# Kernel optimization log

Hardware: AMD Instinct MI355X
Metric: run time of the kernel (lower is better)

## Reference

```python
import jax, jax.numpy as jnp
import numpy as np

D_MODEL = 2048
N_HEADS = 16
N_KV_HEADS = 4
HEAD_DIM = D_MODEL // N_HEADS
KV_DIM = N_KV_HEADS * HEAD_DIM
EPS = 1e-6


def setup_inputs() -> dict:
    key = jax.random.key(0)
    ks = jax.random.split(key, 5)
    N, L = 4, 2048
    x = jax.random.normal(ks[0], (N, L, D_MODEL), dtype=jnp.float32)
    Wqkv = jax.random.normal(ks[1], (D_MODEL, D_MODEL + 2 * KV_DIM), dtype=jnp.float32) * (1.0 / np.sqrt(D_MODEL))
    bqkv = jnp.zeros((D_MODEL + 2 * KV_DIM,), dtype=jnp.float32)
    Wout = jax.random.normal(ks[2], (D_MODEL, D_MODEL), dtype=jnp.float32) * (1.0 / np.sqrt(D_MODEL))
    bout = jnp.zeros((D_MODEL,), dtype=jnp.float32)
    q_scale = jnp.ones((HEAD_DIM,), dtype=jnp.float32)
    k_scale = jnp.ones((HEAD_DIM,), dtype=jnp.float32)
    return {"x": x, "Wqkv": Wqkv, "bqkv": bqkv, "q_scale": q_scale, "k_scale": k_scale, "Wout": Wout, "bout": bout}


def _rmsnorm(x, scale):
    return x * (scale / jnp.sqrt(jnp.mean(jnp.square(x), axis=-1, keepdims=True) + EPS))


def reference(x, Wqkv, bqkv, q_scale, k_scale, Wout, bout):
    N, L, D = x.shape
    qkv = x @ Wqkv + bqkv  # [N, L, D + 2*kv_dim]
    q = qkv[..., :D].reshape(N, L, N_HEADS, HEAD_DIM).transpose(0, 2, 1, 3)          # [N,H,L,hd]
    k = qkv[..., D:D + KV_DIM].reshape(N, L, N_KV_HEADS, HEAD_DIM).transpose(0, 2, 1, 3)  # [N,Hkv,L,hd]
    v = qkv[..., D + KV_DIM:].reshape(N, L, N_KV_HEADS, HEAD_DIM).transpose(0, 2, 1, 3)
    q = _rmsnorm(q, q_scale)
    k = _rmsnorm(k, k_scale)
    # GQA expand (repeat_interleave over head dim)
    n_rep = N_HEADS // N_KV_HEADS
    k = jnp.repeat(k, n_rep, axis=1)
    v = jnp.repeat(v, n_rep, axis=1)
    scale = 1.0 / jnp.sqrt(jnp.float32(HEAD_DIM))
    scores = jnp.einsum("nhqd,nhkd->nhqk", q, k) * scale  # [N,H,L,L]
    causal = jnp.tril(jnp.ones((L, L), dtype=bool))
    scores = jnp.where(causal, scores, jnp.finfo(scores.dtype).min)
    attn = jax.nn.softmax(scores, axis=-1)
    y = jnp.einsum("nhqk,nhkd->nhqd", attn, v)  # [N,H,L,hd]
    y = y.transpose(0, 2, 1, 3).reshape(N, L, D)
    return y @ Wout + bout
```

## Files before the change

### kernel.cpp

```cpp
#include <hip/hip_runtime.h>

typedef unsigned int uint_t;
typedef unsigned short ushort_t;

using f32x4 = __attribute__((ext_vector_type(4))) float;
using bf16x8 = __attribute__((ext_vector_type(8))) short;

#define D_MODEL 2048
#define N_HEADS 16
#define N_KV    4
#define HD      128
#define KV_DIM  (N_KV * HD)
#define NQKV    (D_MODEL + 2*KV_DIM)
#define SEQ     2048
#define NB      4
#define MROWS   (NB * SEQ)
#define SM_SCALE 0.08838834764831845f

__device__ __forceinline__ ushort_t f2bf(float f) {
    uint_t u = __float_as_uint(f);
    u = (u + 0x7FFFu + ((u >> 16) & 1u)) >> 16;
    return (ushort_t)u;
}

__device__ __forceinline__ void gload16(const ushort_t* g, ushort_t* l) {
    __builtin_amdgcn_global_load_lds(
        (const __attribute__((address_space(1))) unsigned int*)g,
        (__attribute__((address_space(3))) unsigned int*)l, 16, 0, 0);
}

__global__ __launch_bounds__(256) void conv_x_kernel(const float* __restrict__ in,
                                                     ushort_t* __restrict__ out, int n) {
    int i = (blockIdx.x * 256 + threadIdx.x) * 4;
    if (i >= n) return;
    float4 v = *(const float4*)&in[i];
    ushort_t o[4] = {f2bf(v.x), f2bf(v.y), f2bf(v.z), f2bf(v.w)};
    *(uint2*)&out[i] = *(uint2*)o;
}

__global__ __launch_bounds__(256) void conv_wt_kernel(const float* __restrict__ W,
                                                      ushort_t* __restrict__ WT,
                                                      int K, int Nout) {
    __shared__ float tile[32][33];
    int n0 = blockIdx.x * 32, k0 = blockIdx.y * 32;
    int tx = threadIdx.x, ty = threadIdx.y;
    for (int i = 0; i < 4; ++i)
        tile[ty + 8*i][tx] = W[(size_t)(k0 + ty + 8*i) * Nout + n0 + tx];
    __syncthreads();
    for (int i = 0; i < 4; ++i)
        WT[(size_t)(n0 + ty + 8*i) * K + k0 + tx] = f2bf(tile[tx][ty + 8*i]);
}

#define GEMM_STAGE(A, BT, k0, b)                                                   \
    for (int i = 0; i < 4; ++i) {                                                  \
        int ci = (w * 4 + i) * 64 + lane;                                          \
        int row = ci >> 3, c = ci & 7, cg = c ^ (row & 7);                         \
        gload16(&A [(size_t)(bm + row) * K + (k0) + cg * 8], &As[b][0][0] + (w * 4 + i) * 512); \
        gload16(&BT[(size_t)(bn + row) * K + (k0) + cg * 8], &Bs[b][0][0] + (w * 4 + i) * 512); \
    }

#define GEMM_MAIN_LOOP(A, BT, K)                                                   \
    GEMM_STAGE(A, BT, 0, 0)                                                        \
    {                                                                              \
        int buf = 0;                                                               \
        for (int k0 = 0; k0 < K; k0 += 64) {                                       \
            __syncthreads();                     \
            if (k0 + 64 < K) { GEMM_STAGE(A, BT, k0 + 64, buf ^ 1) }               \
            for (int kk = 0; kk < 64; kk += 32) {                                  \
                bf16x8 af[4], bfr[4];                                              \
                int k4 = kk >> 3;                                                  \
                for (int i = 0; i < 4; ++i)                                        \
                    af[i]  = *(const bf16x8*)&As[buf][mb + i * 16 + r][((k4 + quad) ^ (r & 7)) * 8]; \
                for (int j = 0; j < 4; ++j)                                        \
                    bfr[j] = *(const bf16x8*)&Bs[buf][nb + j * 16 + r][((k4 + quad) ^ (r & 7)) * 8]; \
                for (int i = 0; i < 4; ++i)                                        \
                    for (int j = 0; j < 4; ++j)                                    \
                        acc[i][j] = __builtin_amdgcn_mfma_f32_16x16x32_bf16(af[i], bfr[j], acc[i][j], 0, 0, 0); \
            }                                                                      \
            buf ^= 1;                                                              \
        }                                                                          \
    }

__global__ __launch_bounds__(256) void gemm_bt_kernel(const ushort_t* __restrict__ A,
                                                      const ushort_t* __restrict__ BT,
                                                      const float* __restrict__ bias,
                                                      float* __restrict__ C,
                                                      int M, int N, int K) {
    __shared__ ushort_t As[2][128][64];
    __shared__ ushort_t Bs[2][128][64];
    const int bm = blockIdx.x * 128, bn = blockIdx.y * 128;
    const int t = threadIdx.x;
    const int w = t >> 6, lane = t & 63, quad = lane >> 4, r = lane & 15;
    const int mb = (w >> 1) * 64, nb = (w & 1) * 64;
    f32x4 acc[4][4] = {};
    GEMM_MAIN_LOOP(A, BT, K)
    for (int i = 0; i < 4; ++i)
        for (int j = 0; j < 4; ++j)
            for (int reg = 0; reg < 4; ++reg) {
                int row = bm + mb + i * 16 + quad * 4 + reg;
                int col = bn + nb + j * 16 + r;
                C[(size_t)row * N + col] = acc[i][j][reg] + bias[col];
            }
}

__global__ __launch_bounds__(256) void gemm_qkv_kernel(const ushort_t* __restrict__ A,
                                                       const ushort_t* __restrict__ BT,
                                                       const float* __restrict__ bias,
                                                       const float* __restrict__ q_scale,
                                                       const float* __restrict__ k_scale,
                                                       ushort_t* __restrict__ Q,
                                                       ushort_t* __restrict__ Kb,
                                                       ushort_t* __restrict__ Vt) {
    __shared__ ushort_t As[2][128][64];
    __shared__ ushort_t Bs[2][128][64];
    const int K = D_MODEL;
    const int bm = blockIdx.x * 128, bn = blockIdx.y * 128;
    const int t = threadIdx.x;
    const int w = t >> 6, lane = t & 63, quad = lane >> 4, r = lane & 15;
    const int mb = (w >> 1) * 64, nb = (w & 1) * 64;
    f32x4 acc[4][4] = {};
    GEMM_MAIN_LOOP(A, BT, K)

    const int g = blockIdx.y;
    float bj[4];
    for (int j = 0; j < 4; ++j) bj[j] = bias[bn + nb + j * 16 + r];
    for (int i = 0; i < 4; ++i)
        for (int j = 0; j < 4; ++j)
            for (int reg = 0; reg < 4; ++reg) acc[i][j][reg] += bj[j];

    const int n = bm >> 11, lb = bm & 2047;
    if (g < 20) {
        __syncthreads();
        float* ssum = (float*)&As[0][0][0];
        for (int i = 0; i < 4; ++i)
            for (int reg = 0; reg < 4; ++reg) {
                float p = 0.f;
                for (int j = 0; j < 4; ++j) p += acc[i][j][reg] * acc[i][j][reg];
                p += __shfl_xor(p, 1); p += __shfl_xor(p, 2);
                p += __shfl_xor(p, 4); p += __shfl_xor(p, 8);
                if (r == 0) ssum[(w & 1) * 128 + mb + i * 16 + quad * 4 + reg] = p;
            }
        __syncthreads();
        const float* scp = (g < 16) ? q_scale : k_scale;
        const float smul = (g < 16) ? SM_SCALE : 1.0f;
        float scj[4];
        for (int j = 0; j < 4; ++j) scj[j] = scp[nb + j * 16 + r];
        ushort_t* dst = (g < 16) ? (Q  + (size_t)(n * 16 + g) * SEQ * HD)
                                 : (Kb + (size_t)(n * 4 + g - 16) * SEQ * HD);
        for (int i = 0; i < 4; ++i)
            for (int reg = 0; reg < 4; ++reg) {
                int rl = mb + i * 16 + quad * 4 + reg;
                float ss = ssum[rl] + ssum[128 + rl];
                float iv = rsqrtf(ss * (1.0f / 128.0f) + 1e-6f) * smul;
                size_t lrow = lb + rl;
                for (int j = 0; j < 4; ++j) {
                    int d = nb + j * 16 + r;
                    dst[lrow * HD + d] = f2bf(acc[i][j][reg] * iv * scj[j]);
                }
            }
    } else {
        ushort_t* dstT = Vt + (size_t)(n * 4 + g - 20) * HD * SEQ;
        for (int i = 0; i < 4; ++i)
            for (int j = 0; j < 4; ++j) {
                int d = nb + j * 16 + r;
                ushort_t o[4];
                for (int reg = 0; reg < 4; ++reg) o[reg] = f2bf(acc[i][j][reg]);
                *(uint2*)&dstT[(size_t)d * SEQ + lb + mb + i * 16 + quad * 4] = *(uint2*)o;
            }
    }
}

__global__ __launch_bounds__(256, 2) void attn_kernel(const ushort_t* __restrict__ Q,
                                                      const ushort_t* __restrict__ K,
                                                      const ushort_t* __restrict__ Vt,
                                                      ushort_t* __restrict__ Y) {
    const int pid = blockIdx.x, h = blockIdx.y, n = blockIdx.z;
    const int kvh = h >> 2;
    const ushort_t* Qp = Q  + (size_t)(n * N_HEADS + h) * SEQ * HD;
    const ushort_t* Kp = K  + (size_t)(n * N_KV + kvh) * SEQ * HD;
    const ushort_t* Vp = Vt + (size_t)(n * N_KV + kvh) * HD * SEQ;

    __shared__ ushort_t Ks[2][64][128];
    __shared__ ushort_t Vts[2][128][64];
    __shared__ ushort_t Ps[128][64];

    const int t = threadIdx.x, w = t >> 6, lane = t & 63, quad = lane >> 4, r = lane & 15;

#define ATTN_STAGE(ct, b)                                                           \
    for (int i = 0; i < 4; ++i) {                                                   \
        int ci = (w * 4 + i) * 64 + lane;                                           \
        {                                         \
            int row = ci >> 4, c = ci & 15, cg = c ^ (row & 7);                     \
            gload16(&Kp[(size_t)((ct) * 64 + row) * HD + cg * 8],                   \
                    &Ks[b][0][0] + (w * 4 + i) * 512);                              \
        }                                                                           \
        {                                         \
            int row = ci >> 3, c = ci & 7, cg = c ^ (row & 7);                      \
            gload16(&Vp[(size_t)row * SEQ + (ct) * 64 + cg * 8],                    \
                    &Vts[b][0][0] + (w * 4 + i) * 512);                             \
        }                                                                           \
    }

    for (int rep = 0; rep < 2; ++rep) {
        const int qt = rep ? (15 - pid) : pid;
        const int q0 = qt * 128;

        __syncthreads();
        ATTN_STAGE(0, 0)

        bf16x8 aq[2][4];
        for (int s = 0; s < 2; ++s)
            for (int kc = 0; kc < 4; ++kc)
                aq[s][kc] = *(const bf16x8*)&Qp[(size_t)(q0 + w * 32 + s * 16 + r) * HD + kc * 32 + quad * 8];

        f32x4 oacc[2][8] = {};
        float lsum[2][4] = {};
        const int nct = 2 * qt + 2;
        int buf = 0;

        for (int ct = 0; ct < nct; ++ct) {
            __syncthreads();
            if (ct + 1 < nct) { ATTN_STAGE(ct + 1, buf ^ 1) }

            if (ct * 64 <= q0 + w * 32 + 31) {
                f32x4 sacc[2][4] = {};
                for (int kc = 0; kc < 4; ++kc)
                    for (int jt = 0; jt < 4; ++jt) {
                        bf16x8 bk = *(const bf16x8*)&Ks[buf][jt * 16 + r][((kc * 4 + quad) ^ (r & 7)) * 8];
                        sacc[0][jt] = __builtin_amdgcn_mfma_f32_16x16x32_bf16(aq[0][kc], bk, sacc[0][jt], 0, 0, 0);
                        sacc[1][jt] = __builtin_amdgcn_mfma_f32_16x16x32_bf16(aq[1][kc], bk, sacc[1][jt], 0, 0, 0);
                    }

                const bool diag = (ct >= 2 * qt);
                for (int s = 0; s < 2; ++s)
                    for (int reg = 0; reg < 4; ++reg) {
                        int prow = w * 32 + s * 16 + quad * 4 + reg;
                        int qg = q0 + prow;
                        float rs = 0.f;
                        for (int jt = 0; jt < 4; ++jt) {
                            float sv = sacc[s][jt][reg];
                            if (diag && (ct * 64 + jt * 16 + r) > qg) sv = -1e30f;
                            float p = __expf(sv);
                            rs += p;
                            int colp = ((((jt * 2 + (r >> 3)) ^ prow) & 7) << 3) | (r & 7);
                            Ps[prow][colp] = (ushort_t)(__float_as_uint(p) >> 16);
                        }
                        lsum[s][reg] += rs;
                    }

                for (int kk = 0; kk < 64; kk += 32) {
                    bf16x8 pa[2];
                    for (int s = 0; s < 2; ++s) {
                        int row = w * 32 + s * 16 + r;
                        pa[s] = *(const bf16x8*)&Ps[row][((((kk >> 3) + quad) ^ row) & 7) * 8];
                    }
                    for (int dt = 0; dt < 8; ++dt) {
                        bf16x8 bv = *(const bf16x8*)&Vts[buf][dt * 16 + r][((((kk >> 3) + quad) ^ (r & 7)) & 7) * 8];
                        oacc[0][dt] = __builtin_amdgcn_mfma_f32_16x16x32_bf16(pa[0], bv, oacc[0][dt], 0, 0, 0);
                        oacc[1][dt] = __builtin_amdgcn_mfma_f32_16x16x32_bf16(pa[1], bv, oacc[1][dt], 0, 0, 0);
                    }
                }
            }
            buf ^= 1;
        }

        for (int s = 0; s < 2; ++s)
            for (int reg = 0; reg < 4; ++reg) {
                float sv = lsum[s][reg];
                for (int m = 1; m < 16; m <<= 1) sv += __shfl_xor(sv, m);
                float invl = 1.0f / sv;
                int lrow = q0 + w * 32 + s * 16 + quad * 4 + reg;
                size_t base = ((size_t)(n * SEQ + lrow)) * D_MODEL + h * HD;
                for (int dt = 0; dt < 8; ++dt)
                    Y[base + dt * 16 + r] = f2bf(oacc[s][dt][reg] * invl);
            }
    }
#undef ATTN_STAGE
}

extern "C" void kernel_launch(void* const* d_in, const int* in_sizes, int n_in,
                              void* d_out, int out_size, void* d_ws, size_t ws_size,
                              hipStream_t stream) {
    const float* x       = (const float*)d_in[0];
    const float* Wqkv    = (const float*)d_in[1];
    const float* bqkv    = (const float*)d_in[2];
    const float* q_scale = (const float*)d_in[3];
    const float* k_scale = (const float*)d_in[4];
    const float* Wout    = (const float*)d_in[5];
    const float* bout    = (const float*)d_in[6];
    float* out = (float*)d_out;

    ushort_t* xb  = (ushort_t*)d_ws;
    ushort_t* WT  = xb  + (size_t)MROWS * D_MODEL;
    ushort_t* Qb  = WT  + (size_t)NQKV * D_MODEL;
    ushort_t* Kb  = Qb  + (size_t)NB * N_HEADS * SEQ * HD;
    ushort_t* Vtb = Kb  + (size_t)NB * N_KV * SEQ * HD;

    conv_x_kernel<<<MROWS * D_MODEL / 1024, 256, 0, stream>>>(x, xb, MROWS * D_MODEL);
    conv_wt_kernel<<<dim3(NQKV / 32, D_MODEL / 32), dim3(32, 8), 0, stream>>>(Wqkv, WT, D_MODEL, NQKV);
    gemm_qkv_kernel<<<dim3(MROWS / 128, NQKV / 128), 256, 0, stream>>>(xb, WT, bqkv, q_scale, k_scale, Qb, Kb, Vtb);
    conv_wt_kernel<<<dim3(D_MODEL / 32, D_MODEL / 32), dim3(32, 8), 0, stream>>>(Wout, WT, D_MODEL, D_MODEL);
    attn_kernel<<<dim3(8, N_HEADS, NB), 256, 0, stream>>>(Qb, Kb, Vtb, xb);
    gemm_bt_kernel<<<dim3(MROWS / 128, D_MODEL / 128), 256, 0, stream>>>(xb, WT, bout, out, MROWS, D_MODEL, D_MODEL);
}
```

Measured before the change: 454.1 us.

## Rewrite GEMMs with 256x256 tiles, 8 waves and split-K pipelined staging

Both projection GEMMs move from 128x128 tiles with 4 waves to 256x256 tiles with 8 waves (512 threads). Each K tile is split into two 32-wide halves that load directly into LDS, with explicit vmcnt waits, raw s_barrier and s_setprio around the MFMA bursts so loads overlap compute. The aim is more operand reuse per LDS byte and less global traffic per FLOP. The QKV epilogue is remapped so each block covers two heads, keeping the fused RMSNorm and V-transpose. In exchange there are far fewer blocks, which may leave CUs idle, and the hand-counted waits are a correctness risk.

```diff
diff --git a/kernel.cpp b/kernel.cpp
--- a/kernel.cpp
+++ b/kernel.cpp
@@ -15,6 +15,7 @@
 #define SEQ     2048
 #define NB      4
 #define MROWS   (NB * SEQ)
+#define NKT     32
 #define SM_SCALE 0.08838834764831845f
 
 __device__ __forceinline__ ushort_t f2bf(float f) {
@@ -28,6 +29,8 @@
         (const __attribute__((address_space(1))) unsigned int*)g,
         (__attribute__((address_space(3))) unsigned int*)l, 16, 0, 0);
 }
+
+#define VMCNT(N) asm volatile("s_waitcnt vmcnt(" #N ")" ::: "memory")
 
 __global__ __launch_bounds__(256) void conv_x_kernel(const float* __restrict__ in,
                                                      ushort_t* __restrict__ out, int n) {
@@ -51,121 +54,154 @@
         WT[(size_t)(n0 + ty + 8*i) * K + k0 + tx] = f2bf(tile[tx][ty + 8*i]);
 }
 
-#define GEMM_STAGE(A, BT, k0, b)                                                   \
-    for (int i = 0; i < 4; ++i) {                                                  \
-        int ci = (w * 4 + i) * 64 + lane;                                          \
-        int row = ci >> 3, c = ci & 7, cg = c ^ (row & 7);                         \
-        gload16(&A [(size_t)(bm + row) * K + (k0) + cg * 8], &As[b][0][0] + (w * 4 + i) * 512); \
-        gload16(&BT[(size_t)(bn + row) * K + (k0) + cg * 8], &Bs[b][0][0] + (w * 4 + i) * 512); \
-    }
-
-#define GEMM_MAIN_LOOP(A, BT, K)                                                   \
-    GEMM_STAGE(A, BT, 0, 0)                                                        \
+#define G256_PRELUDE                                                               \
+    const int t = threadIdx.x;                                                     \
+    const int wid = t >> 6, lane = t & 63, quad = lane >> 4, r = lane & 15;        \
+    const int wr = wid >> 2, wc = wid & 3;                                         \
+    int srow[2], skc[2], sdst[2];                                                  \
+    for (int l = 0; l < 2; ++l) {                                                  \
+        int u = l * 512 + t, lrow = u >> 3, cc = (u & 7) ^ (lrow & 7);             \
+        srow[l] = lrow * 2 + (cc >> 2); skc[l] = (cc & 3) * 8; sdst[l] = u * 8;    \
+    }                                                                              \
+    const int swz  = ((((r & 1) << 2) | quad) ^ ((r >> 1) & 7)) * 8;               \
+    const int aoff = (wr * 64 + (r >> 1)) * 64 + swz;                              \
+    const int boff = (wc * 32 + (r >> 1)) * 64 + swz;                              \
+    f32x4 acc[8][4] = {};                                                          \
+    bf16x8 bfr[4];
+
+#define STAGE1(PTR, ROWBASE, kt, kh, DST, dbuf)                                    \
+    if ((kt) < NKT) {                                                              \
+        for (int l = 0; l < 2; ++l)                                                \
+            gload16(&PTR[(size_t)((ROWBASE) + srow[l]) * 2048 +                    \
+                         (kt) * 64 + (kh) * 32 + skc[l]],                          \
+                    &DST[dbuf][kh][0] + sdst[l]);                                  \
+    }
+
+#define PHASE(buf, kh, mh, STAGE_STMT, VM_STMT)                                    \
     {                                                                              \
-        int buf = 0;                                                               \
-        for (int k0 = 0; k0 < K; k0 += 64) {                                       \
-            __syncthreads();                     \
-            if (k0 + 64 < K) { GEMM_STAGE(A, BT, k0 + 64, buf ^ 1) }               \
-            for (int kk = 0; kk < 64; kk += 32) {                                  \
-                bf16x8 af[4], bfr[4];                                              \
-                int k4 = kk >> 3;                                                  \
-                for (int i = 0; i < 4; ++i)                                        \
-                    af[i]  = *(const bf16x8*)&As[buf][mb + i * 16 + r][((k4 + quad) ^ (r & 7)) * 8]; \
-                for (int j = 0; j < 4; ++j)                                        \
-                    bfr[j] = *(const bf16x8*)&Bs[buf][nb + j * 16 + r][((k4 + quad) ^ (r & 7)) * 8]; \
-                for (int i = 0; i < 4; ++i)                                        \
-                    for (int j = 0; j < 4; ++j)                                    \
-                        acc[i][j] = __builtin_amdgcn_mfma_f32_16x16x32_bf16(af[i], bfr[j], acc[i][j], 0, 0, 0); \
-            }                                                                      \
-            buf ^= 1;                                                              \
-        }                                                                          \
-    }
-
-__global__ __launch_bounds__(256) void gemm_bt_kernel(const ushort_t* __restrict__ A,
-                                                      const ushort_t* __restrict__ BT,
-                                                      const float* __restrict__ bias,
-                                                      float* __restrict__ C,
-                                                      int M, int N, int K) {
-    __shared__ ushort_t As[2][128][64];
-    __shared__ ushort_t Bs[2][128][64];
-    const int bm = blockIdx.x * 128, bn = blockIdx.y * 128;
-    const int t = threadIdx.x;
-    const int w = t >> 6, lane = t & 63, quad = lane >> 4, r = lane & 15;
-    const int mb = (w >> 1) * 64, nb = (w & 1) * 64;
-    f32x4 acc[4][4] = {};
-    GEMM_MAIN_LOOP(A, BT, K)
-    for (int i = 0; i < 4; ++i)
-        for (int j = 0; j < 4; ++j)
+        bf16x8 af[4];                                                              \
+        for (int i = 0; i < 4; ++i)                                                \
+            af[i] = *(const bf16x8*)&As[buf][kh][aoff + ((mh) * 4 + i) * 512];     \
+        if ((mh) == 0)                                                             \
+            for (int jf = 0; jf < 4; ++jf)                                         \
+                bfr[jf] = *(const bf16x8*)&Bs[buf][kh][boff + jf * 512];           \
+        STAGE_STMT;                                                                \
+        __builtin_amdgcn_s_barrier();                                              \
+        __builtin_amdgcn_s_setprio(1);                                             \
+        for (int i = 0; i < 4; ++i)                                                \
+            for (int jf = 0; jf < 4; ++jf)                                         \
+                acc[(mh) * 4 + i][jf] = __builtin_amdgcn_mfma_f32_16x16x32_bf16(   \
+                    af[i], bfr[jf], acc[(mh) * 4 + i][jf], 0, 0, 0);               \
+        __builtin_amdgcn_s_setprio(0);                                             \
+        VM_STMT;                                                                   \
+        __builtin_amdgcn_s_barrier();                                              \
+    }
+
+#define KTILE(j, buf)                                                              \
+    PHASE(buf, 0, 0, STAGE1(Aptr, bm, (j) + 1, 1, As, (buf) ^ 1), ;)               \
+    PHASE(buf, 0, 1, STAGE1(Bptr, bn, (j) + 1, 1, Bs, (buf) ^ 1),                  \
+          { if ((j) + 1 < NKT) { VMCNT(8); } else { VMCNT(0); } })                 \
+    PHASE(buf, 1, 0, STAGE1(Aptr, bm, (j) + 2, 0, As, buf), ;)                     \
+    PHASE(buf, 1, 1, STAGE1(Bptr, bn, (j) + 2, 0, Bs, buf),                        \
+          { if ((j) + 2 < NKT) { VMCNT(8); }                                       \
+            else if ((j) + 1 < NKT) { VMCNT(4); }                                  \
+            else { VMCNT(0); } })
+
+#define G256_MAIN_LOOP                                                             \
+    STAGE1(Aptr, bm, 0, 0, As, 0);                                                 \
+    STAGE1(Bptr, bn, 0, 0, Bs, 0);                                                 \
+    STAGE1(Aptr, bm, 0, 1, As, 0);                                                 \
+    STAGE1(Bptr, bn, 0, 1, Bs, 0);                                                 \
+    STAGE1(Aptr, bm, 1, 0, As, 1);                                                 \
+    STAGE1(Bptr, bn, 1, 0, Bs, 1);                                                 \
+    VMCNT(8);                                                                      \
+    __builtin_amdgcn_s_barrier();                                                  \
+    _Pragma("unroll 1")                                                            \
+    for (int j = 0; j < NKT; j += 2) {                                             \
+        KTILE(j, 0)                                                                \
+        KTILE(j + 1, 1)                                                            \
+    }
+
+__global__ __launch_bounds__(512, 2) void gemm_bt_kernel(const ushort_t* __restrict__ Aptr,
+                                                         const ushort_t* __restrict__ Bptr,
+                                                         const float* __restrict__ bias,
+                                                         float* __restrict__ C,
+                                                         int M, int N, int K) {
+    __shared__ __align__(16) ushort_t As[2][2][128 * 64];
+    __shared__ __align__(16) ushort_t Bs[2][2][128 * 64];
+    const int bm = blockIdx.x * 256, bn = blockIdx.y * 256;
+    G256_PRELUDE
+    G256_MAIN_LOOP
+    for (int i = 0; i < 8; ++i)
+        for (int jf = 0; jf < 4; ++jf) {
+            int col = bn + wc * 64 + jf * 16 + r;
+            float bv = bias[col];
             for (int reg = 0; reg < 4; ++reg) {
-                int row = bm + mb + i * 16 + quad * 4 + reg;
-                int col = bn + nb + j * 16 + r;
-                C[(size_t)row * N + col] = acc[i][j][reg] + bias[col];
-            }
-}
-
-__global__ __launch_bounds__(256) void gemm_qkv_kernel(const ushort_t* __restrict__ A,
-                                                       const ushort_t* __restrict__ BT,
-                                                       const float* __restrict__ bias,
-                                                       const float* __restrict__ q_scale,
-                                                       const float* __restrict__ k_scale,
-                                                       ushort_t* __restrict__ Q,
-                                                       ushort_t* __restrict__ Kb,
-                                                       ushort_t* __restrict__ Vt) {
-    __shared__ ushort_t As[2][128][64];
-    __shared__ ushort_t Bs[2][128][64];
-    const int K = D_MODEL;
-    const int bm = blockIdx.x * 128, bn = blockIdx.y * 128;
-    const int t = threadIdx.x;
-    const int w = t >> 6, lane = t & 63, quad = lane >> 4, r = lane & 15;
-    const int mb = (w >> 1) * 64, nb = (w & 1) * 64;
-    f32x4 acc[4][4] = {};
-    GEMM_MAIN_LOOP(A, BT, K)
+                int row = bm + wr * 128 + i * 16 + quad * 4 + reg;
+                C[(size_t)row * N + col] = acc[i][jf][reg] + bv;
+            }
+        }
+}
+
+__global__ __launch_bounds__(512, 2) void gemm_qkv_kernel(const ushort_t* __restrict__ Aptr,
+                                                          const ushort_t* __restrict__ Bptr,
+                                                          const float* __restrict__ bias,
+                                                          const float* __restrict__ q_scale,
+                                                          const float* __restrict__ k_scale,
+                                                          ushort_t* __restrict__ Q,
+                                                          ushort_t* __restrict__ Kb,
+                                                          ushort_t* __restrict__ Vt) {
+    __shared__ __align__(16) ushort_t As[2][2][128 * 64];
+    __shared__ __align__(16) ushort_t Bs[2][2][128 * 64];
+    const int bm = blockIdx.x * 256, bn = blockIdx.y * 256;
+    G256_PRELUDE
+    G256_MAIN_LOOP
 
     const int g = blockIdx.y;
     float bj[4];
-    for (int j = 0; j < 4; ++j) bj[j] = bias[bn + nb + j * 16 + r];
-    for (int i = 0; i < 4; ++i)
-        for (int j = 0; j < 4; ++j)
-            for (int reg = 0; reg < 4; ++reg) acc[i][j][reg] += bj[j];
+    for (int jf = 0; jf < 4; ++jf) bj[jf] = bias[bn + wc * 64 + jf * 16 + r];
+    for (int i = 0; i < 8; ++i)
+        for (int jf = 0; jf < 4; ++jf)
+            for (int reg = 0; reg < 4; ++reg) acc[i][jf][reg] += bj[jf];
 
     const int n = bm >> 11, lb = bm & 2047;
-    if (g < 20) {
-        __syncthreads();
+    const int hh = wc >> 1, dbase = (wc & 1) * 64;
+    if (g < 10) {
         float* ssum = (float*)&As[0][0][0];
-        for (int i = 0; i < 4; ++i)
+        for (int i = 0; i < 8; ++i)
             for (int reg = 0; reg < 4; ++reg) {
                 float p = 0.f;
-                for (int j = 0; j < 4; ++j) p += acc[i][j][reg] * acc[i][j][reg];
+                for (int jf = 0; jf < 4; ++jf) p += acc[i][jf][reg] * acc[i][jf][reg];
                 p += __shfl_xor(p, 1); p += __shfl_xor(p, 2);
                 p += __shfl_xor(p, 4); p += __shfl_xor(p, 8);
-                if (r == 0) ssum[(w & 1) * 128 + mb + i * 16 + quad * 4 + reg] = p;
+                if (r == 0)
+                    ssum[(((wr * 2 + hh) * 2) + (wc & 1)) * 128 + i * 16 + quad * 4 + reg] = p;
             }
         __syncthreads();
-        const float* scp = (g < 16) ? q_scale : k_scale;
-        const float smul = (g < 16) ? SM_SCALE : 1.0f;
+        const float* scp = (g < 8) ? q_scale : k_scale;
+        const float smul = (g < 8) ? SM_SCALE : 1.0f;
         float scj[4];
-        for (int j = 0; j < 4; ++j) scj[j] = scp[nb + j * 16 + r];
-        ushort_t* dst = (g < 16) ? (Q  + (size_t)(n * 16 + g) * SEQ * HD)
-                                 : (Kb + (size_t)(n * 4 + g - 16) * SEQ * HD);
-        for (int i = 0; i < 4; ++i)
+        for (int jf = 0; jf < 4; ++jf) scj[jf] = scp[dbase + jf * 16 + r];
+        ushort_t* dst = (g < 8) ? (Q  + (size_t)(n * 16 + g * 2 + hh) * SEQ * HD)
+                                : (Kb + (size_t)(n * 4 + (g - 8) * 2 + hh) * SEQ * HD);
+        const int sbase = ((wr * 2 + hh) * 2) * 128;
+        for (int i = 0; i < 8; ++i)
             for (int reg = 0; reg < 4; ++reg) {
-                int rl = mb + i * 16 + quad * 4 + reg;
-                float ss = ssum[rl] + ssum[128 + rl];
+                int rl = i * 16 + quad * 4 + reg;
+                float ss = ssum[sbase + rl] + ssum[sbase + 128 + rl];
                 float iv = rsqrtf(ss * (1.0f / 128.0f) + 1e-6f) * smul;
-                size_t lrow = lb + rl;
-                for (int j = 0; j < 4; ++j) {
-                    int d = nb + j * 16 + r;
-                    dst[lrow * HD + d] = f2bf(acc[i][j][reg] * iv * scj[j]);
-                }
+                size_t lrow = lb + wr * 128 + rl;
+                for (int jf = 0; jf < 4; ++jf)
+                    dst[lrow * HD + dbase + jf * 16 + r] = f2bf(acc[i][jf][reg] * iv * scj[jf]);
             }
     } else {
-        ushort_t* dstT = Vt + (size_t)(n * 4 + g - 20) * HD * SEQ;
-        for (int i = 0; i < 4; ++i)
-            for (int j = 0; j < 4; ++j) {
-                int d = nb + j * 16 + r;
+        ushort_t* dstT = Vt + (size_t)(n * 4 + (g - 10) * 2 + hh) * HD * SEQ;
+        for (int i = 0; i < 8; ++i)
+            for (int jf = 0; jf < 4; ++jf) {
+                int d = dbase + jf * 16 + r;
                 ushort_t o[4];
-                for (int reg = 0; reg < 4; ++reg) o[reg] = f2bf(acc[i][j][reg]);
-                *(uint2*)&dstT[(size_t)d * SEQ + lb + mb + i * 16 + quad * 4] = *(uint2*)o;
+                for (int reg = 0; reg < 4; ++reg) o[reg] = f2bf(acc[i][jf][reg]);
+                *(uint2*)&dstT[(size_t)d * SEQ + lb + wr * 128 + i * 16 + quad * 4] = *(uint2*)o;
             }
     }
 }
@@ -298,8 +334,8 @@
 
     conv_x_kernel<<<MROWS * D_MODEL / 1024, 256, 0, stream>>>(x, xb, MROWS * D_MODEL);
     conv_wt_kernel<<<dim3(NQKV / 32, D_MODEL / 32), dim3(32, 8), 0, stream>>>(Wqkv, WT, D_MODEL, NQKV);
-    gemm_qkv_kernel<<<dim3(MROWS / 128, NQKV / 128), 256, 0, stream>>>(xb, WT, bqkv, q_scale, k_scale, Qb, Kb, Vtb);
+    gemm_qkv_kernel<<<dim3(MROWS / 256, NQKV / 256), 512, 0, stream>>>(xb, WT, bqkv, q_scale, k_scale, Qb, Kb, Vtb);
     conv_wt_kernel<<<dim3(D_MODEL / 32, D_MODEL / 32), dim3(32, 8), 0, stream>>>(Wout, WT, D_MODEL, D_MODEL);
     attn_kernel<<<dim3(8, N_HEADS, NB), 256, 0, stream>>>(Qb, Kb, Vtb, xb);
-    gemm_bt_kernel<<<dim3(MROWS / 128, D_MODEL / 128), 256, 0, stream>>>(xb, WT, bout, out, MROWS, D_MODEL, D_MODEL);
-}
+    gemm_bt_kernel<<<dim3(MROWS / 256, D_MODEL / 256), 512, 0, stream>>>(xb, WT, bout, out, MROWS, D_MODEL, D_MODEL);
+}
```

After: 471.7 us. 3.9% more time.

## Replace output GEMM with 256x256 tiled, 512-thread pipelined kernel and add MFMA priority hints

Applied to the files above, without the earlier changes.

Rewrites the output projection GEMM to use 256x256 tiles with 8 waves. Loads are split into half-K stages issued through direct global-to-LDS loads, with explicit vmcnt waits, barriers and a swizzled LDS layout. A block-index remap groups tiles for cache locality. The attention kernel also raises wave priority around its MFMA loops with s_setprio. The intent is more data reuse per tile and better overlap of loads with compute, at the cost of heavier register and LDS use and hand-tuned wait counts that must match the exact number of loads in flight.

```diff
diff --git a/kernel.cpp b/kernel.cpp
--- a/kernel.cpp
+++ b/kernel.cpp
@@ -15,6 +15,7 @@
 #define SEQ     2048
 #define NB      4
 #define MROWS   (NB * SEQ)
+#define NKT     32
 #define SM_SCALE 0.08838834764831845f
 
 __device__ __forceinline__ ushort_t f2bf(float f) {
@@ -28,6 +29,8 @@
         (const __attribute__((address_space(1))) unsigned int*)g,
         (__attribute__((address_space(3))) unsigned int*)l, 16, 0, 0);
 }
+
+#define VMCNT(N) asm volatile("s_waitcnt vmcnt(" #N ")")
 
 __global__ __launch_bounds__(256) void conv_x_kernel(const float* __restrict__ in,
                                                      ushort_t* __restrict__ out, int n) {
@@ -81,28 +84,6 @@
         }                                                                          \
     }
 
-__global__ __launch_bounds__(256) void gemm_bt_kernel(const ushort_t* __restrict__ A,
-                                                      const ushort_t* __restrict__ BT,
-                                                      const float* __restrict__ bias,
-                                                      float* __restrict__ C,
-                                                      int M, int N, int K) {
-    __shared__ ushort_t As[2][128][64];
-    __shared__ ushort_t Bs[2][128][64];
-    const int bm = blockIdx.x * 128, bn = blockIdx.y * 128;
-    const int t = threadIdx.x;
-    const int w = t >> 6, lane = t & 63, quad = lane >> 4, r = lane & 15;
-    const int mb = (w >> 1) * 64, nb = (w & 1) * 64;
-    f32x4 acc[4][4] = {};
-    GEMM_MAIN_LOOP(A, BT, K)
-    for (int i = 0; i < 4; ++i)
-        for (int j = 0; j < 4; ++j)
-            for (int reg = 0; reg < 4; ++reg) {
-                int row = bm + mb + i * 16 + quad * 4 + reg;
-                int col = bn + nb + j * 16 + r;
-                C[(size_t)row * N + col] = acc[i][j][reg] + bias[col];
-            }
-}
-
 __global__ __launch_bounds__(256) void gemm_qkv_kernel(const ushort_t* __restrict__ A,
                                                        const ushort_t* __restrict__ BT,
                                                        const float* __restrict__ bias,
@@ -170,6 +151,97 @@
     }
 }
 
+#define G256_PRELUDE                                                               \
+    const int t = threadIdx.x;                                                     \
+    const int wid = t >> 6, lane = t & 63, quad = lane >> 4, r = lane & 15;        \
+    const int wr = wid >> 2, wc = wid & 3;                                         \
+    int srow[2], skc[2], sdst[2];                                                  \
+    for (int l = 0; l < 2; ++l) {                                                  \
+        int u = l * 512 + t, lrow = u >> 3, cc = (u & 7) ^ (lrow & 7);             \
+        srow[l] = lrow * 2 + (cc >> 2); skc[l] = (cc & 3) * 8; sdst[l] = u * 8;    \
+    }                                                                              \
+    const int swz  = ((((r & 1) << 2) | quad) ^ ((r >> 1) & 7)) * 8;               \
+    const int aoff = (wr * 64 + (r >> 1)) * 64 + swz;                              \
+    const int boff = (wc * 32 + (r >> 1)) * 64 + swz;                              \
+    f32x4 acc[8][4] = {};                                                          \
+    bf16x8 bfr[4];
+
+#define STAGE1(PTR, ROWBASE, kt, kh, DST, dbuf)                                    \
+    if ((kt) < NKT) {                                                              \
+        for (int l = 0; l < 2; ++l)                                                \
+            gload16(&PTR[(size_t)((ROWBASE) + srow[l]) * 2048 +                    \
+                         (kt) * 64 + (kh) * 32 + skc[l]],                          \
+                    &DST[dbuf][kh][0] + sdst[l]);                                  \
+    }
+
+#define PHASE(buf, kh, mh, STAGE_STMT, VM_STMT)                                    \
+    {                                                                              \
+        bf16x8 af[4];                                                              \
+        for (int i = 0; i < 4; ++i)                                                \
+            af[i] = *(const bf16x8*)&As[buf][kh][aoff + ((mh) * 4 + i) * 512];     \
+        if ((mh) == 0)                                                             \
+            for (int jf = 0; jf < 4; ++jf)                                         \
+                bfr[jf] = *(const bf16x8*)&Bs[buf][kh][boff + jf * 512];           \
+        STAGE_STMT;                                                                \
+        __builtin_amdgcn_s_barrier();                                              \
+        __builtin_amdgcn_s_setprio(1);                                             \
+        for (int i = 0; i < 4; ++i)                                                \
+            for (int jf = 0; jf < 4; ++jf)                                         \
+                acc[(mh) * 4 + i][jf] = __builtin_amdgcn_mfma_f32_16x16x32_bf16(   \
+                    af[i], bfr[jf], acc[(mh) * 4 + i][jf], 0, 0, 0);               \
+        __builtin_amdgcn_s_setprio(0);                                             \
+        VM_STMT;                                                                   \
+        __builtin_amdgcn_s_barrier();                                              \
+    }
+
+#define KTILE(j, buf)                                                              \
+    PHASE(buf, 0, 0, STAGE1(Aptr, bm, (j) + 1, 1, As, (buf) ^ 1), ;)               \
+    PHASE(buf, 0, 1, STAGE1(Bptr, bn, (j) + 1, 1, Bs, (buf) ^ 1),                  \
+          { if ((j) + 1 < NKT) { VMCNT(8); } else { VMCNT(0); } })                 \
+    PHASE(buf, 1, 0, STAGE1(Aptr, bm, (j) + 2, 0, As, buf), ;)                     \
+    PHASE(buf, 1, 1, STAGE1(Bptr, bn, (j) + 2, 0, Bs, buf),                        \
+          { if ((j) + 2 < NKT) { VMCNT(8); }                                       \
+            else if ((j) + 1 < NKT) { VMCNT(4); }                                  \
+            else { VMCNT(0); } })
+
+#define G256_MAIN_LOOP                                                             \
+    STAGE1(Aptr, bm, 0, 0, As, 0);                                                 \
+    STAGE1(Bptr, bn, 0, 0, Bs, 0);                                                 \
+    STAGE1(Aptr, bm, 0, 1, As, 0);                                                 \
+    STAGE1(Bptr, bn, 0, 1, Bs, 0);                                                 \
+    STAGE1(Aptr, bm, 1, 0, As, 1);                                                 \
+    STAGE1(Bptr, bn, 1, 0, Bs, 1);                                                 \
+    VMCNT(8);                                                                      \
+    __builtin_amdgcn_s_barrier();                                                  \
+    _Pragma("unroll 1")                                                            \
+    for (int j = 0; j < NKT; j += 2) {                                             \
+        KTILE(j, 0)                                                                \
+        KTILE(j + 1, 1)                                                            \
+    }
+
+__global__ __launch_bounds__(512, 2) void gemm_bt_kernel(const ushort_t* __restrict__ Aptr,
+                                                         const ushort_t* __restrict__ Bptr,
+                                                         const float* __restrict__ bias,
+                                                         float* __restrict__ C,
+                                                         int M, int N, int K) {
+    __shared__ __align__(16) ushort_t As[2][2][128 * 64];
+    __shared__ __align__(16) ushort_t Bs[2][2][128 * 64];
+    const int lin = blockIdx.y * 32 + blockIdx.x;
+    const int nl  = (lin & 7) * 32 + (lin >> 3);
+    const int bm = (nl & 31) * 256, bn = (nl >> 5) * 256;
+    G256_PRELUDE
+    G256_MAIN_LOOP
+    for (int i = 0; i < 8; ++i)
+        for (int jf = 0; jf < 4; ++jf) {
+            int col = bn + wc * 64 + jf * 16 + r;
+            float bv = bias[col];
+            for (int reg = 0; reg < 4; ++reg) {
+                int row = bm + wr * 128 + i * 16 + quad * 4 + reg;
+                C[(size_t)row * N + col] = acc[i][jf][reg] + bv;
+            }
+        }
+}
+
 __global__ __launch_bounds__(256, 2) void attn_kernel(const ushort_t* __restrict__ Q,
                                                       const ushort_t* __restrict__ K,
                                                       const ushort_t* __restrict__ Vt,
@@ -224,12 +296,14 @@
 
             if (ct * 64 <= q0 + w * 32 + 31) {
                 f32x4 sacc[2][4] = {};
+                __builtin_amdgcn_s_setprio(1);
                 for (int kc = 0; kc < 4; ++kc)
                     for (int jt = 0; jt < 4; ++jt) {
                         bf16x8 bk = *(const bf16x8*)&Ks[buf][jt * 16 + r][((kc * 4 + quad) ^ (r & 7)) * 8];
                         sacc[0][jt] = __builtin_amdgcn_mfma_f32_16x16x32_bf16(aq[0][kc], bk, sacc[0][jt], 0, 0, 0);
                         sacc[1][jt] = __builtin_amdgcn_mfma_f32_16x16x32_bf16(aq[1][kc], bk, sacc[1][jt], 0, 0, 0);
                     }
+                __builtin_amdgcn_s_setprio(0);
 
                 const bool diag = (ct >= 2 * qt);
                 for (int s = 0; s < 2; ++s)
@@ -248,6 +322,7 @@
                         lsum[s][reg] += rs;
                     }
 
+                __builtin_amdgcn_s_setprio(1);
                 for (int kk = 0; kk < 64; kk += 32) {
                     bf16x8 pa[2];
                     for (int s = 0; s < 2; ++s) {
@@ -260,6 +335,7 @@
                         oacc[1][dt] = __builtin_amdgcn_mfma_f32_16x16x32_bf16(pa[1], bv, oacc[1][dt], 0, 0, 0);
                     }
                 }
+                __builtin_amdgcn_s_setprio(0);
             }
             buf ^= 1;
         }
@@ -301,5 +377,5 @@
     gemm_qkv_kernel<<<dim3(MROWS / 128, NQKV / 128), 256, 0, stream>>>(xb, WT, bqkv, q_scale, k_scale, Qb, Kb, Vtb);
     conv_wt_kernel<<<dim3(D_MODEL / 32, D_MODEL / 32), dim3(32, 8), 0, stream>>>(Wout, WT, D_MODEL, D_MODEL);
     attn_kernel<<<dim3(8, N_HEADS, NB), 256, 0, stream>>>(Qb, Kb, Vtb, xb);
-    gemm_bt_kernel<<<dim3(MROWS / 128, D_MODEL / 128), 256, 0, stream>>>(xb, WT, bout, out, MROWS, D_MODEL, D_MODEL);
-}
+    gemm_bt_kernel<<<dim3(MROWS / 256, D_MODEL / 256), 512, 0, stream>>>(xb, WT, bout, out, MROWS, D_MODEL, D_MODEL);
+}
```

Result: no change. 455.9 us (+0.4%).

## Transpose QK^T MFMA output to pack P writes and simplify row sums

Applied to the files above, without the earlier changes.

The attention kernel swaps the MFMA operand order so each lane holds four consecutive keys for one query row. This lets P be packed into 64-bit LDS stores instead of scalar 16-bit stores, and the row-sum reduction shrinks to two shuffles per row. The normalizer is later broadcast back to the output layout with a shuffle. Separately, the x conversion kernel now processes 8 floats per thread with 128-bit stores. The new P swizzle must still line up with the read side, and that carries correctness risk.

```diff
diff --git a/kernel.cpp b/kernel.cpp
--- a/kernel.cpp
+++ b/kernel.cpp
@@ -31,11 +31,13 @@
 
 __global__ __launch_bounds__(256) void conv_x_kernel(const float* __restrict__ in,
                                                      ushort_t* __restrict__ out, int n) {
-    int i = (blockIdx.x * 256 + threadIdx.x) * 4;
+    int i = (blockIdx.x * 256 + threadIdx.x) * 8;
     if (i >= n) return;
-    float4 v = *(const float4*)&in[i];
-    ushort_t o[4] = {f2bf(v.x), f2bf(v.y), f2bf(v.z), f2bf(v.w)};
-    *(uint2*)&out[i] = *(uint2*)o;
+    float4 v0 = *(const float4*)&in[i];
+    float4 v1 = *(const float4*)&in[i + 4];
+    ushort_t o[8] = {f2bf(v0.x), f2bf(v0.y), f2bf(v0.z), f2bf(v0.w),
+                     f2bf(v1.x), f2bf(v1.y), f2bf(v1.z), f2bf(v1.w)};
+    *(uint4*)&out[i] = *(uint4*)o;
 }
 
 __global__ __launch_bounds__(256) void conv_wt_kernel(const float* __restrict__ W,
@@ -214,7 +216,7 @@
                 aq[s][kc] = *(const bf16x8*)&Qp[(size_t)(q0 + w * 32 + s * 16 + r) * HD + kc * 32 + quad * 8];
 
         f32x4 oacc[2][8] = {};
-        float lsum[2][4] = {};
+        float lsum[2] = {};
         const int nct = 2 * qt + 2;
         int buf = 0;
 
@@ -227,32 +229,43 @@
                 for (int kc = 0; kc < 4; ++kc)
                     for (int jt = 0; jt < 4; ++jt) {
                         bf16x8 bk = *(const bf16x8*)&Ks[buf][jt * 16 + r][((kc * 4 + quad) ^ (r & 7)) * 8];
-                        sacc[0][jt] = __builtin_amdgcn_mfma_f32_16x16x32_bf16(aq[0][kc], bk, sacc[0][jt], 0, 0, 0);
-                        sacc[1][jt] = __builtin_amdgcn_mfma_f32_16x16x32_bf16(aq[1][kc], bk, sacc[1][jt], 0, 0, 0);
+                        sacc[0][jt] = __builtin_amdgcn_mfma_f32_16x16x32_bf16(bk, aq[0][kc], sacc[0][jt], 0, 0, 0);
+                        sacc[1][jt] = __builtin_amdgcn_mfma_f32_16x16x32_bf16(bk, aq[1][kc], sacc[1][jt], 0, 0, 0);
                     }
 
                 const bool diag = (ct >= 2 * qt);
-                for (int s = 0; s < 2; ++s)
-                    for (int reg = 0; reg < 4; ++reg) {
-                        int prow = w * 32 + s * 16 + quad * 4 + reg;
-                        int qg = q0 + prow;
-                        float rs = 0.f;
-                        for (int jt = 0; jt < 4; ++jt) {
-                            float sv = sacc[s][jt][reg];
-                            if (diag && (ct * 64 + jt * 16 + r) > qg) sv = -1e30f;
-                            float p = __expf(sv);
-                            rs += p;
-                            int colp = ((((jt * 2 + (r >> 3)) ^ prow) & 7) << 3) | (r & 7);
-                            Ps[prow][colp] = (ushort_t)(__float_as_uint(p) >> 16);
+                for (int s = 0; s < 2; ++s) {
+                    const int qg = q0 + w * 32 + s * 16 + r;
+                    const int prow = w * 32 + s * 16 + r;
+                    float rs = 0.f;
+                    for (int jt = 0; jt < 4; ++jt) {
+                        uint_t pk[2];
+                        for (int pr = 0; pr < 2; ++pr) {
+                            float e[2];
+                            for (int u = 0; u < 2; ++u) {
+                                int reg = pr * 2 + u;
+                                int key = ct * 64 + jt * 16 + quad * 4 + reg;
+                                float sv = sacc[s][jt][reg];
+                                if (diag && key > qg) sv = -1e30f;
+                                e[u] = __expf(sv);
+                                rs += e[u];
+                            }
+                            pk[pr] = (__float_as_uint(e[0]) >> 16) |
+                                     (__float_as_uint(e[1]) & 0xFFFF0000u);
                         }
-                        lsum[s][reg] += rs;
+                        int cc = (jt * 4 + quad) ^ ((r & 7) << 1);
+                        *(uint2*)&Ps[prow][cc * 4] = make_uint2(pk[0], pk[1]);
                     }
+                    lsum[s] += rs;
+                }
 
                 for (int kk = 0; kk < 64; kk += 32) {
+                    const int kb = kk >> 5;
                     bf16x8 pa[2];
                     for (int s = 0; s < 2; ++s) {
-                        int row = w * 32 + s * 16 + r;
-                        pa[s] = *(const bf16x8*)&Ps[row][((((kk >> 3) + quad) ^ row) & 7) * 8];
+                        int prow = w * 32 + s * 16 + r;
+                        int cc = (kb * 8 + quad * 2) ^ ((r & 7) << 1);
+                        pa[s] = *(const bf16x8*)&Ps[prow][cc * 4];
                     }
                     for (int dt = 0; dt < 8; ++dt) {
                         bf16x8 bv = *(const bf16x8*)&Vts[buf][dt * 16 + r][((((kk >> 3) + quad) ^ (r & 7)) & 7) * 8];
@@ -264,16 +277,19 @@
             buf ^= 1;
         }
 
-        for (int s = 0; s < 2; ++s)
+        for (int s = 0; s < 2; ++s) {
+            float ls = lsum[s];
+            ls += __shfl_xor(ls, 16);
+            ls += __shfl_xor(ls, 32);
+            float inv = 1.0f / ls;
             for (int reg = 0; reg < 4; ++reg) {
-                float sv = lsum[s][reg];
-                for (int m = 1; m < 16; m <<= 1) sv += __shfl_xor(sv, m);
-                float invl = 1.0f / sv;
+                float invl = __shfl(inv, quad * 4 + reg);
                 int lrow = q0 + w * 32 + s * 16 + quad * 4 + reg;
                 size_t base = ((size_t)(n * SEQ + lrow)) * D_MODEL + h * HD;
                 for (int dt = 0; dt < 8; ++dt)
                     Y[base + dt * 16 + r] = f2bf(oacc[s][dt][reg] * invl);
             }
+        }
     }
 #undef ATTN_STAGE
 }
@@ -296,7 +312,7 @@
     ushort_t* Kb  = Qb  + (size_t)NB * N_HEADS * SEQ * HD;
     ushort_t* Vtb = Kb  + (size_t)NB * N_KV * SEQ * HD;
 
-    conv_x_kernel<<<MROWS * D_MODEL / 1024, 256, 0, stream>>>(x, xb, MROWS * D_MODEL);
+    conv_x_kernel<<<MROWS * D_MODEL / 2048, 256, 0, stream>>>(x, xb, MROWS * D_MODEL);
     conv_wt_kernel<<<dim3(NQKV / 32, D_MODEL / 32), dim3(32, 8), 0, stream>>>(Wqkv, WT, D_MODEL, NQKV);
     gemm_qkv_kernel<<<dim3(MROWS / 128, NQKV / 128), 256, 0, stream>>>(xb, WT, bqkv, q_scale, k_scale, Qb, Kb, Vtb);
     conv_wt_kernel<<<dim3(D_MODEL / 32, D_MODEL / 32), dim3(32, 8), 0, stream>>>(Wout, WT, D_MODEL, D_MODEL);
```

After: 451.4 us. No clear change (-0.6%).
